# Kernel optimization log

Hardware: AMD Instinct MI355X
Metric: run time of the kernel (lower is better)

Reference implementation:

```python
import jax, jax.numpy as jnp
import numpy as np

D_MODEL = 1024
N_HEADS = 16
HEAD_DIM = D_MODEL // N_HEADS
D_FF = 4 * D_MODEL


def _layernorm(x, g, b, eps=1e-5):
    mu = jnp.mean(x, axis=-1, keepdims=True)
    var = jnp.var(x, axis=-1, keepdims=True)
    return (x - mu) * jax.lax.rsqrt(var + eps) * g + b


def setup_inputs() -> dict:
    key = jax.random.key(0)
    ks = jax.random.split(key, 12)
    s = lambda fan_in: 1.0 / np.sqrt(fan_in)
    x = jax.random.normal(ks[0], (2, 2048, D_MODEL), dtype=jnp.float32)
    return {
        "x": x,
        "ln1_g": jnp.ones((D_MODEL,), jnp.float32),
        "ln1_b": jnp.zeros((D_MODEL,), jnp.float32),
        "w_qkv": jax.random.uniform(ks[1], (D_MODEL, 3 * D_MODEL), jnp.float32, -s(D_MODEL), s(D_MODEL)),
        "b_qkv": jax.random.uniform(ks[2], (3 * D_MODEL,), jnp.float32, -s(D_MODEL), s(D_MODEL)),
        "w_out": jax.random.uniform(ks[3], (D_MODEL, D_MODEL), jnp.float32, -s(D_MODEL), s(D_MODEL)),
        "b_out": jax.random.uniform(ks[4], (D_MODEL,), jnp.float32, -s(D_MODEL), s(D_MODEL)),
        "ln2_g": jnp.ones((D_MODEL,), jnp.float32),
        "ln2_b": jnp.zeros((D_MODEL,), jnp.float32),
        "w_ff1": jax.random.uniform(ks[5], (D_MODEL, D_FF), jnp.float32, -s(D_MODEL), s(D_MODEL)),
        "b_ff1": jax.random.uniform(ks[6], (D_FF,), jnp.float32, -s(D_MODEL), s(D_MODEL)),
        "w_ff2": jax.random.uniform(ks[7], (D_FF, D_MODEL), jnp.float32, -s(D_FF), s(D_FF)),
        "b_ff2": jax.random.uniform(ks[8], (D_MODEL,), jnp.float32, -s(D_FF), s(D_FF)),
    }


def reference(x, ln1_g, ln1_b, w_qkv, b_qkv, w_out, b_out,
              ln2_g, ln2_b, w_ff1, b_ff1, w_ff2, b_ff2):
    B, T, C = x.shape
    # --- pre-LN causal self-attention + residual ---
    h = _layernorm(x, ln1_g, ln1_b)
    qkv = h @ w_qkv + b_qkv                                  # [B,T,3C]
    qkv = qkv.reshape(B, T, 3, N_HEADS, HEAD_DIM)
    q, k, v = qkv[:, :, 0], qkv[:, :, 1], qkv[:, :, 2]       # [B,T,H,Dh]
    scores = jnp.einsum("bthd,bshd->bhts", q, k) / np.sqrt(HEAD_DIM).astype(np.float32)
    causal = jnp.tril(jnp.ones((T, T), dtype=bool))
    scores = jnp.where(causal, scores, -jnp.inf)
    weights = jax.nn.softmax(scores, axis=-1)                # [B,H,T,T]
    attn = jnp.einsum("bhts,bshd->bthd", weights, v).reshape(B, T, C)
    x = x + attn @ w_out + b_out
    # --- pre-LN GELU FFN + residual ---
    h = _layernorm(x, ln2_g, ln2_b)
    h = jax.nn.gelu(h @ w_ff1 + b_ff1, approximate=False)    # torch GELU = erf
    x = x + h @ w_ff2 + b_ff2
    return x
```

## Files before the change

### kernel.cpp

```cpp
#include <hip/hip_runtime.h>
#include <hip/hip_bf16.h>
#include <math.h>

#define TSEQ 2048
#define BATCH 2
#define CDIM 1024
#define NH 16
#define HD 64
#define DFF 4096
#define ROWS (BATCH*TSEQ)

typedef __attribute__((ext_vector_type(4))) float f32x4;
typedef __attribute__((ext_vector_type(8))) short bf16x8;
typedef __attribute__((ext_vector_type(4))) unsigned short u16x4;

__device__ __forceinline__ void gload_lds16(const void* g, void* l) {
    void* gv = const_cast<void*>(g);
    __builtin_amdgcn_global_load_lds((__attribute__((address_space(1))) void*)gv,
                                     (__attribute__((address_space(3))) void*)l, 16, 0, 0);
}

__device__ __forceinline__ unsigned short f2bf(float f) {
    unsigned int u = __float_as_uint(f);
    return (unsigned short)((u + 0x7FFFu + ((u >> 16) & 1u)) >> 16);
}
__device__ __forceinline__ float bf2f(unsigned short u) {
    return __uint_as_float((unsigned int)u << 16);
}
__device__ __forceinline__ unsigned int cvt_pk_bf16(float lo, float hi) {
    unsigned int r;
    asm("v_cvt_pk_bf16_f32 %0, %1, %2" : "=v"(r) : "v"(lo), "v"(hi));
    return r;
}
__device__ __forceinline__ float fast_gelu(float v) {
    float u = fmaf(0.044715f * v * v, v, v);
    float e = __expf(-1.5957691216057308f * u);
    return v * __builtin_amdgcn_rcpf(1.0f + e);
}

__global__ __launch_bounds__(256) void ln_kernel(const float* __restrict__ x,
                                                 const float* __restrict__ g,
                                                 const float* __restrict__ b,
                                                 unsigned short* __restrict__ out) {
    int row = blockIdx.x;
    int tid = threadIdx.x;
    const float* xr = x + (size_t)row * CDIM;
    float4 v = *(const float4*)(xr + tid * 4);
    float s  = v.x + v.y + v.z + v.w;
    float s2 = v.x*v.x + v.y*v.y + v.z*v.z + v.w*v.w;
    #pragma unroll
    for (int off = 32; off >= 1; off >>= 1) {
        s  += __shfl_down(s, off);
        s2 += __shfl_down(s2, off);
    }
    __shared__ float red[8];
    int wid = tid >> 6, lane = tid & 63;
    if (lane == 0) { red[wid] = s; red[wid + 4] = s2; }
    __syncthreads();
    float ts  = red[0] + red[1] + red[2] + red[3];
    float ts2 = red[4] + red[5] + red[6] + red[7];
    float mu  = ts * (1.0f / CDIM);
    float var = ts2 * (1.0f / CDIM) - mu * mu;
    float rstd = rsqrtf(var + 1e-5f);
    float4 gv = *(const float4*)(g + tid * 4);
    float4 bv = *(const float4*)(b + tid * 4);
    unsigned short o4[4];
    o4[0] = f2bf((v.x - mu) * rstd * gv.x + bv.x);
    o4[1] = f2bf((v.y - mu) * rstd * gv.y + bv.y);
    o4[2] = f2bf((v.z - mu) * rstd * gv.z + bv.z);
    o4[3] = f2bf((v.w - mu) * rstd * gv.w + bv.w);
    *(u16x4*)(out + (size_t)row * CDIM + tid * 4) = *(u16x4*)o4;
}

__global__ __launch_bounds__(256) void transpose_cast_kernel(const float* __restrict__ W,
                                                             unsigned short* __restrict__ Wt,
                                                             int K, int N) {
    __shared__ float T[64][65];
    int tid = threadIdx.x;
    int n0 = blockIdx.x * 64, k0 = blockIdx.y * 64;
    int kr = tid >> 4;
    int nc = (tid & 15) * 4;
    #pragma unroll
    for (int i = 0; i < 4; ++i) {
        float4 v = *(const float4*)&W[(size_t)(k0 + kr + i*16) * N + (n0 + nc)];
        T[kr + i*16][nc + 0] = v.x;
        T[kr + i*16][nc + 1] = v.y;
        T[kr + i*16][nc + 2] = v.z;
        T[kr + i*16][nc + 3] = v.w;
    }
    __syncthreads();
    int n  = tid >> 2;
    int kb = (tid & 3) * 16;
    unsigned short tmp[16];
    #pragma unroll
    for (int i = 0; i < 16; ++i) tmp[i] = f2bf(T[kb + i][n]);
    unsigned short* dst = Wt + (size_t)(n0 + n) * K + (k0 + kb);
    *(int4*)dst       = *(int4*)&tmp[0];
    *(int4*)(dst + 8) = *(int4*)&tmp[8];
}

__global__ __launch_bounds__(256) void kvfrag_kernel(const unsigned short* __restrict__ qkv,
                                                     unsigned short* __restrict__ kfrag,
                                                     unsigned short* __restrict__ vfrag) {
    __shared__ unsigned short Kt[64][72];
    __shared__ unsigned short Vt[64][72];
    const int tid = threadIdx.x;
    const int j  = blockIdx.x;
    const int bh = blockIdx.y;
    const int b = bh >> 4, h = bh & 15;
    {
        const int r  = tid >> 2;
        const int c0 = (tid & 3) * 16;
        const unsigned short* src = qkv + ((size_t)(b * TSEQ + j * 64 + r)) * 3072 + 1024 + h * 64 + c0;
        bf16x8 k0 = *(const bf16x8*)src;
        bf16x8 k1 = *(const bf16x8*)(src + 8);
        bf16x8 v0 = *(const bf16x8*)(src + 1024);
        bf16x8 v1 = *(const bf16x8*)(src + 1032);
        *(bf16x8*)&Kt[r][c0]     = k0;
        *(bf16x8*)&Kt[r][c0 + 8] = k1;
        *(bf16x8*)&Vt[r][c0]     = v0;
        *(bf16x8*)&Vt[r][c0 + 8] = v1;
    }
    __syncthreads();
    const int l  = tid & 63;
    const int qd = tid >> 6;
    const size_t tbase = ((size_t)(bh * 32 + j)) * 8 * 512;
    #pragma unroll
    for (int pass = 0; pass < 2; ++pass) {
        const int kc = qd + pass * 4;
        const int sb = kc >> 1, g = kc & 1;
        bf16x8 kv = *(const bf16x8*)&Kt[sb * 16 + (l & 15)][g * 32 + (l >> 4) * 8];
        *(bf16x8*)(kfrag + tbase + kc * 512 + l * 8) = kv;

        const int vc = qd + pass * 4;
        const int kb = vc >> 2, db = vc & 3;
        unsigned short tmp[8];
        #pragma unroll
        for (int i = 0; i < 8; ++i)
            tmp[i] = Vt[kb * 32 + (l >> 4) * 8 + i][db * 16 + (l & 15)];
        *(bf16x8*)(vfrag + tbase + vc * 512 + l * 8) = *(bf16x8*)tmp;
    }
}

template<int EPI>
__global__ __launch_bounds__(256) void gemm_kernel(const unsigned short* __restrict__ A,
                                                   const unsigned short* __restrict__ Bt,
                                                   const float* __restrict__ bias,
                                                   const float* __restrict__ res,
                                                   void* __restrict__ Cout,
                                                   int M, int N, int K, int nbx, int rpx) {
    __shared__ __align__(16) unsigned short As[3 * 4096];
    __shared__ __align__(16) unsigned short Bs[3 * 4096];
    const int tid = threadIdx.x;
    const int l   = tid & 63;
    const int w   = tid >> 6;
    const int wr  = (w >> 1) * 64;
    const int wc  = (w & 1) * 64;
    const int lin = blockIdx.x;
    const int xcd = lin & 7;
    const int idx = lin >> 3;
    const long brow = (long)(xcd * rpx + idx / nbx) * 128;
    const long bcol = (long)(idx % nbx) * 128;

    const int srow = tid >> 2;
    const int schk = ((tid & 3) ^ ((srow >> 1) & 3)) * 8;
    const unsigned short* gA = A  + (size_t)(brow + srow) * K + schk;
    const unsigned short* gB = Bt + (size_t)(bcol + srow) * K + schk;

    f32x4 acc[4][4];
    #pragma unroll
    for (int m = 0; m < 4; ++m)
        #pragma unroll
        for (int n = 0; n < 4; ++n) acc[m][n] = (f32x4){0.f, 0.f, 0.f, 0.f};

    #define STAGE128(buf, koff_)                                                       \
        do {                                                                           \
            unsigned short* lA_ = As + (buf) * 4096 + tid * 8;                         \
            unsigned short* lB_ = Bs + (buf) * 4096 + tid * 8;                         \
            gload_lds16(gA + (koff_), lA_);                                            \
            gload_lds16(gA + (size_t)64 * K + (koff_), lA_ + 2048);                    \
            gload_lds16(gB + (koff_), lB_);                                            \
            gload_lds16(gB + (size_t)64 * K + (koff_), lB_ + 2048);                    \
        } while (0)

    STAGE128(0, 0);
    STAGE128(1, 32);

    int cur = 0;
    for (int k0 = 0; k0 < K; k0 += 32) {
        if (k0 + 32 < K) asm volatile("s_waitcnt vmcnt(4)" ::: "memory");
        else             asm volatile("s_waitcnt vmcnt(0)" ::: "memory");
        __builtin_amdgcn_s_barrier();
        asm volatile("" ::: "memory");

        const unsigned short* cA = As + cur * 4096 + (wr >> 6) * 2048;
        const unsigned short* cB = Bs + cur * 4096 + (wc >> 6) * 2048;
        const int koff = ((l >> 4) ^ (((l & 15) >> 1) & 3)) * 8;
        bf16x8 af[4], bf[4];
        #pragma unroll
        for (int m = 0; m < 4; ++m)
            af[m] = *(const bf16x8*)&cA[(m * 16 + (l & 15)) * 32 + koff];
        #pragma unroll
        for (int n = 0; n < 4; ++n)
            bf[n] = *(const bf16x8*)&cB[(n * 16 + (l & 15)) * 32 + koff];
        __builtin_amdgcn_s_setprio(1);
        #pragma unroll
        for (int m = 0; m < 4; ++m)
            #pragma unroll
            for (int n = 0; n < 4; ++n)
                acc[m][n] = __builtin_amdgcn_mfma_f32_16x16x32_bf16(af[m], bf[n], acc[m][n], 0, 0, 0);
        __builtin_amdgcn_s_setprio(0);

        if (k0 + 64 < K) {
            int nxt = cur + 2; if (nxt >= 3) nxt -= 3;
            STAGE128(nxt, k0 + 64);
        }
        cur = cur + 1; if (cur == 3) cur = 0;
    }
    #undef STAGE128

    #pragma unroll
    for (int m = 0; m < 4; ++m) {
        const int rown = wr + m * 16 + (l >> 4) * 4;
        #pragma unroll
        for (int n = 0; n < 4; ++n) {
            const long col = bcol + wc + n * 16 + (l & 15);
            const float bb = bias[col];
            #pragma unroll
            for (int r = 0; r < 4; ++r) {
                const long row = brow + rown + r;
                float v = acc[m][n][r] + bb;
                if (EPI == 1) {
                    v += res[row * N + col];
                    ((float*)Cout)[row * N + col] = v;
                } else if (EPI == 2) {
                    ((unsigned short*)Cout)[row * N + col] = f2bf(fast_gelu(v));
                } else {
                    ((unsigned short*)Cout)[row * N + col] = f2bf(v);
                }
            }
        }
    }
}

template<int EPI>
__global__ __launch_bounds__(256) void gemm64_kernel(const unsigned short* __restrict__ A,
                                                     const unsigned short* __restrict__ Bt,
                                                     const float* __restrict__ bias,
                                                     const float* __restrict__ res,
                                                     void* __restrict__ Cout,
                                                     int M, int N, int K, int nbx, int rpx) {
    __shared__ __align__(16) unsigned short As[3 * 64 * 64];
    __shared__ __align__(16) unsigned short Bs[3 * 128 * 64];
    const int tid = threadIdx.x;
    const int l   = tid & 63;
    const int w   = tid >> 6;
    const int wr  = (w >> 1) * 32;
    const int wc  = (w & 1) * 64;
    const int lin = blockIdx.x;
    const int xcd = lin & 7;
    const int idx = lin >> 3;
    const long brow = (long)(xcd * rpx + idx / nbx) * 64;
    const long bcol = (long)(idx % nbx) * 128;

    const int srow = tid >> 3;
    const int schk = ((tid & 7) ^ (srow & 7)) * 8;
    const unsigned short* gA = A  + (size_t)(brow + srow) * K + schk;
    const unsigned short* gB = Bt + (size_t)(bcol + srow) * K + schk;

    f32x4 acc[2][4];
    #pragma unroll
    for (int m = 0; m < 2; ++m)
        #pragma unroll
        for (int n = 0; n < 4; ++n) acc[m][n] = (f32x4){0.f, 0.f, 0.f, 0.f};

    #define STAGE64(buf, koff_)                                                        \
        do {                                                                           \
            unsigned short* lA_ = As + (buf) * 4096 + tid * 8;                         \
            unsigned short* lB_ = Bs + (buf) * 8192 + tid * 8;                         \
            _Pragma("unroll")                                                          \
            for (int p = 0; p < 2; ++p)                                                \
                gload_lds16(gA + (size_t)(32 * p) * K + (koff_), lA_ + p * 2048);      \
            _Pragma("unroll")                                                          \
            for (int p = 0; p < 4; ++p)                                                \
                gload_lds16(gB + (size_t)(32 * p) * K + (koff_), lB_ + p * 2048);      \
        } while (0)

    STAGE64(0, 0);
    STAGE64(1, 64);

    int cur = 0;
    for (int k0 = 0; k0 < K; k0 += 64) {
        if (k0 + 64 < K) asm volatile("s_waitcnt vmcnt(6)" ::: "memory");
        else             asm volatile("s_waitcnt vmcnt(0)" ::: "memory");
        __builtin_amdgcn_s_barrier();
        asm volatile("" ::: "memory");

        const unsigned short* cA = As + cur * 4096;
        const unsigned short* cB = Bs + cur * 8192;
        #pragma unroll
        for (int gg = 0; gg < 2; ++gg) {
            const int koff = ((gg * 4 + (l >> 4)) ^ (l & 7)) * 8;
            bf16x8 af[2], bf[4];
            #pragma unroll
            for (int m = 0; m < 2; ++m)
                af[m] = *(const bf16x8*)&cA[(wr + m * 16 + (l & 15)) * 64 + koff];
            #pragma unroll
            for (int n = 0; n < 4; ++n)
                bf[n] = *(const bf16x8*)&cB[(wc + n * 16 + (l & 15)) * 64 + koff];
            __builtin_amdgcn_s_setprio(1);
            #pragma unroll
            for (int m = 0; m < 2; ++m)
                #pragma unroll
                for (int n = 0; n < 4; ++n)
                    acc[m][n] = __builtin_amdgcn_mfma_f32_16x16x32_bf16(af[m], bf[n], acc[m][n], 0, 0, 0);
            __builtin_amdgcn_s_setprio(0);
        }

        if (k0 + 128 < K) {
            int nxt = cur + 2; if (nxt >= 3) nxt -= 3;
            STAGE64(nxt, k0 + 128);
        }
        cur = cur + 1; if (cur == 3) cur = 0;
    }
    #undef STAGE64

    #pragma unroll
    for (int m = 0; m < 2; ++m) {
        const int rown = wr + m * 16 + (l >> 4) * 4;
        #pragma unroll
        for (int n = 0; n < 4; ++n) {
            const long col = bcol + wc + n * 16 + (l & 15);
            const float bb = bias[col];
            #pragma unroll
            for (int r = 0; r < 4; ++r) {
                const long row = brow + rown + r;
                float v = acc[m][n][r] + bb;
                if (EPI == 1) {
                    v += res[row * N + col];
                    ((float*)Cout)[row * N + col] = v;
                } else if (EPI == 2) {
                    ((unsigned short*)Cout)[row * N + col] = f2bf(fast_gelu(v));
                } else {
                    ((unsigned short*)Cout)[row * N + col] = f2bf(v);
                }
            }
        }
    }
}

#define QSCALE 0.18033688011112042f
__global__ __launch_bounds__(64) void attn_kernel(const unsigned short* __restrict__ qkv,
                                                  const unsigned short* __restrict__ kfrag,
                                                  const unsigned short* __restrict__ vfrag,
                                                  unsigned short* __restrict__ out) {
    __shared__ __align__(16) unsigned short Ps[16 * 128];

    const int l    = threadIdx.x;
    const int q    = l & 15;
    const int g    = l >> 4;
    const int lin  = blockIdx.x;
    const int xcd  = lin & 7;
    const int rest = lin >> 3;
    const int h    = xcd + 8 * (rest & 1);
    const int b    = (rest >> 1) & 1;
    const int strip = 127 - (rest >> 2);
    const int jmax  = strip >> 2;
    const size_t rowbase = (size_t)b * TSEQ;
    const int bh = b * NH + h;
    const int qglob = strip * 16 + q;

    const unsigned short* kfb = kfrag + (size_t)bh * 32 * 8 * 512;
    const unsigned short* vfb = vfrag + (size_t)bh * 32 * 8 * 512;

    bf16x8 aq0, aq1;
    {
        const unsigned short* qp = qkv + (rowbase + qglob) * 3072 + h * 64 + g * 8;
        bf16x8 t0 = *(const bf16x8*)qp;
        bf16x8 t1 = *(const bf16x8*)(qp + 32);
        #pragma unroll
        for (int i = 0; i < 8; ++i) {
            aq0[i] = (short)f2bf(bf2f((unsigned short)t0[i]) * QSCALE);
            aq1[i] = (short)f2bf(bf2f((unsigned short)t1[i]) * QSCALE);
        }
    }

    float mrow = -INFINITY, lrow = 0.f;
    f32x4 o[4];
    #pragma unroll
    for (int d = 0; d < 4; ++d) o[d] = (f32x4){0.f, 0.f, 0.f, 0.f};

    for (int j = 0; j + 1 <= jmax; j += 2) {
        const bool diag2 = (j + 1 == jmax);

        bf16x8 kf[16];
        #pragma unroll
        for (int t = 0; t < 2; ++t)
            #pragma unroll
            for (int sb = 0; sb < 4; ++sb) {
                const unsigned short* kp = kfb + (size_t)((j + t) * 8 + sb * 2) * 512 + l * 8;
                kf[t * 8 + sb * 2]     = *(const bf16x8*)kp;
                kf[t * 8 + sb * 2 + 1] = *(const bf16x8*)(kp + 512);
            }

        f32x4 sf[8];
        __builtin_amdgcn_s_setprio(1);
        #pragma unroll
        for (int t = 0; t < 2; ++t)
            #pragma unroll
            for (int sb = 0; sb < 4; ++sb) {
                f32x4 acc = (f32x4){0.f, 0.f, 0.f, 0.f};
                acc = __builtin_amdgcn_mfma_f32_16x16x32_bf16(kf[t*8 + sb*2],     aq0, acc, 0, 0, 0);
                acc = __builtin_amdgcn_mfma_f32_16x16x32_bf16(kf[t*8 + sb*2 + 1], aq1, acc, 0, 0, 0);
                sf[t*4 + sb] = acc;
            }
        __builtin_amdgcn_s_setprio(0);

        bf16x8 vf[16];
        #pragma unroll
        for (int kb = 0; kb < 4; ++kb)
            #pragma unroll
            for (int db = 0; db < 4; ++db)
                vf[kb * 4 + db] = *(const bf16x8*)(vfb + (size_t)((j + (kb >> 1)) * 8 + (kb & 1) * 4 + db) * 512 + l * 8);

        if (diag2) {
            #pragma unroll
            for (int sb = 0; sb < 4; ++sb) {
                const int sg = (j + 1) * 64 + sb * 16 + 4 * g;
                #pragma unroll
                for (int r = 0; r < 4; ++r)
                    if (sg + r > qglob) sf[4 + sb][r] = -INFINITY;
            }
        }

        f32x4 mv = sf[0];
        #pragma unroll
        for (int i = 1; i < 8; ++i)
            #pragma unroll
            for (int r = 0; r < 4; ++r) mv[r] = fmaxf(mv[r], sf[i][r]);
        float mloc = fmaxf(fmaxf(mv[0], mv[1]), fmaxf(mv[2], mv[3]));
        mloc = fmaxf(mloc, __shfl_xor(mloc, 16));
        mloc = fmaxf(mloc, __shfl_xor(mloc, 32));
        const float mn = fmaxf(mrow, mloc);
        const float alpha = exp2f(mrow - mn);
        mrow = mn;

        float psum = 0.f;
        #pragma unroll
        for (int i = 0; i < 8; ++i) {
            const int t = i >> 2, sb = i & 3;
            float p0 = exp2f(sf[i][0] - mn);
            float p1 = exp2f(sf[i][1] - mn);
            float p2 = exp2f(sf[i][2] - mn);
            float p3 = exp2f(sf[i][3] - mn);
            psum += (p0 + p1) + (p2 + p3);
            unsigned int pk0 = cvt_pk_bf16(p0, p1);
            unsigned int pk1 = cvt_pk_bf16(p2, p3);
            const int c16 = (t * 8 + sb * 2 + (g >> 1)) ^ (q & 7);
            *(uint2*)((char*)Ps + q * 256 + c16 * 16 + (g & 1) * 8) = make_uint2(pk0, pk1);
        }
        psum += __shfl_xor(psum, 16);
        psum += __shfl_xor(psum, 32);
        lrow = lrow * alpha + psum;

        float al[4];
        #pragma unroll
        for (int r = 0; r < 4; ++r) al[r] = __shfl(alpha, g * 4 + r);
        #pragma unroll
        for (int d = 0; d < 4; ++d)
            #pragma unroll
            for (int r = 0; r < 4; ++r) o[d][r] *= al[r];

        __builtin_amdgcn_s_setprio(1);
        #pragma unroll
        for (int kb = 0; kb < 4; ++kb) {
            const int c16 = (kb * 4 + g) ^ (q & 7);
            bf16x8 pa = *(const bf16x8*)((const char*)Ps + q * 256 + c16 * 16);
            #pragma unroll
            for (int db = 0; db < 4; ++db)
                o[db] = __builtin_amdgcn_mfma_f32_16x16x32_bf16(pa, vf[kb * 4 + db], o[db], 0, 0, 0);
        }
        __builtin_amdgcn_s_setprio(0);
    }

    if ((jmax & 1) == 0) {
        const int j = jmax;
        bf16x8 kf[8];
        #pragma unroll
        for (int sb = 0; sb < 4; ++sb) {
            const unsigned short* kp = kfb + (size_t)(j * 8 + sb * 2) * 512 + l * 8;
            kf[sb * 2]     = *(const bf16x8*)kp;
            kf[sb * 2 + 1] = *(const bf16x8*)(kp + 512);
        }
        f32x4 sf[4];
        __builtin_amdgcn_s_setprio(1);
        #pragma unroll
        for (int sb = 0; sb < 4; ++sb) {
            f32x4 acc = (f32x4){0.f, 0.f, 0.f, 0.f};
            acc = __builtin_amdgcn_mfma_f32_16x16x32_bf16(kf[sb*2],     aq0, acc, 0, 0, 0);
            acc = __builtin_amdgcn_mfma_f32_16x16x32_bf16(kf[sb*2 + 1], aq1, acc, 0, 0, 0);
            sf[sb] = acc;
        }
        __builtin_amdgcn_s_setprio(0);

        bf16x8 vf[8];
        #pragma unroll
        for (int kb = 0; kb < 2; ++kb)
            #pragma unroll
            for (int db = 0; db < 4; ++db)
                vf[kb * 4 + db] = *(const bf16x8*)(vfb + (size_t)(j * 8 + kb * 4 + db) * 512 + l * 8);

        #pragma unroll
        for (int sb = 0; sb < 4; ++sb) {
            const int sg = j * 64 + sb * 16 + 4 * g;
            #pragma unroll
            for (int r = 0; r < 4; ++r)
                if (sg + r > qglob) sf[sb][r] = -INFINITY;
        }

        f32x4 mv = sf[0];
        #pragma unroll
        for (int i = 1; i < 4; ++i)
            #pragma unroll
            for (int r = 0; r < 4; ++r) mv[r] = fmaxf(mv[r], sf[i][r]);
        float mloc = fmaxf(fmaxf(mv[0], mv[1]), fmaxf(mv[2], mv[3]));
        mloc = fmaxf(mloc, __shfl_xor(mloc, 16));
        mloc = fmaxf(mloc, __shfl_xor(mloc, 32));
        const float mn = fmaxf(mrow, mloc);
        const float alpha = exp2f(mrow - mn);
        mrow = mn;

        float psum = 0.f;
        #pragma unroll
        for (int sb = 0; sb < 4; ++sb) {
            float p0 = exp2f(sf[sb][0] - mn);
            float p1 = exp2f(sf[sb][1] - mn);
            float p2 = exp2f(sf[sb][2] - mn);
            float p3 = exp2f(sf[sb][3] - mn);
            psum += (p0 + p1) + (p2 + p3);
            unsigned int pk0 = cvt_pk_bf16(p0, p1);
            unsigned int pk1 = cvt_pk_bf16(p2, p3);
            const int c16 = (sb * 2 + (g >> 1)) ^ (q & 7);
            *(uint2*)((char*)Ps + q * 256 + c16 * 16 + (g & 1) * 8) = make_uint2(pk0, pk1);
        }
        psum += __shfl_xor(psum, 16);
        psum += __shfl_xor(psum, 32);
        lrow = lrow * alpha + psum;

        float al[4];
        #pragma unroll
        for (int r = 0; r < 4; ++r) al[r] = __shfl(alpha, g * 4 + r);
        #pragma unroll
        for (int d = 0; d < 4; ++d)
            #pragma unroll
            for (int r = 0; r < 4; ++r) o[d][r] *= al[r];

        __builtin_amdgcn_s_setprio(1);
        #pragma unroll
        for (int kb = 0; kb < 2; ++kb) {
            const int c16 = (kb * 4 + g) ^ (q & 7);
            bf16x8 pa = *(const bf16x8*)((const char*)Ps + q * 256 + c16 * 16);
            #pragma unroll
            for (int db = 0; db < 4; ++db)
                o[db] = __builtin_amdgcn_mfma_f32_16x16x32_bf16(pa, vf[kb * 4 + db], o[db], 0, 0, 0);
        }
        __builtin_amdgcn_s_setprio(0);
    }

    float linv[4];
    #pragma unroll
    for (int r = 0; r < 4; ++r) linv[r] = 1.0f / __shfl(lrow, g * 4 + r);
    #pragma unroll
    for (int r = 0; r < 4; ++r) {
        const size_t rb = (rowbase + strip * 16 + g * 4 + r) * (size_t)CDIM + h * 64 + q;
        #pragma unroll
        for (int d = 0; d < 4; ++d)
            out[rb + d * 16] = f2bf(o[d][r] * linv[r]);
    }
}

extern "C" void kernel_launch(void* const* d_in, const int* in_sizes, int n_in,
                              void* d_out, int out_size, void* d_ws, size_t ws_size,
                              hipStream_t stream) {
    const float* x     = (const float*)d_in[0];
    const float* ln1_g = (const float*)d_in[1];
    const float* ln1_b = (const float*)d_in[2];
    const float* w_qkv = (const float*)d_in[3];
    const float* b_qkv = (const float*)d_in[4];
    const float* w_out = (const float*)d_in[5];
    const float* b_out = (const float*)d_in[6];
    const float* ln2_g = (const float*)d_in[7];
    const float* ln2_b = (const float*)d_in[8];
    const float* w_ff1 = (const float*)d_in[9];
    const float* b_ff1 = (const float*)d_in[10];
    const float* w_ff2 = (const float*)d_in[11];
    const float* b_ff2 = (const float*)d_in[12];
    float* out = (float*)d_out;

    char* wsb = (char*)d_ws;
    unsigned short* h_bf    = (unsigned short*)(wsb);
    unsigned short* qkv_bf  = (unsigned short*)(wsb + 8ll  * 1024 * 1024);
    unsigned short* attn_bf = (unsigned short*)(wsb + 32ll * 1024 * 1024);
    float*          x1      = (float*)         (wsb + 40ll * 1024 * 1024);
    unsigned short* kfrag   = (unsigned short*)(wsb + 40ll * 1024 * 1024);
    unsigned short* vfrag   = (unsigned short*)(wsb + 48ll * 1024 * 1024);
    unsigned short* wqkvT   = (unsigned short*)(wsb + 56ll * 1024 * 1024);
    unsigned short* woutT   = (unsigned short*)(wsb + 62ll * 1024 * 1024);
    unsigned short* wff1T   = (unsigned short*)(wsb + 64ll * 1024 * 1024);
    unsigned short* wff2T   = (unsigned short*)(wsb + 72ll * 1024 * 1024);
    unsigned short* ff1_bf  = (unsigned short*)(wsb + 8ll  * 1024 * 1024);

    transpose_cast_kernel<<<dim3(48, 16), 256, 0, stream>>>(w_qkv, wqkvT, 1024, 3072);
    transpose_cast_kernel<<<dim3(16, 16), 256, 0, stream>>>(w_out, woutT, 1024, 1024);
    transpose_cast_kernel<<<dim3(64, 16), 256, 0, stream>>>(w_ff1, wff1T, 1024, 4096);
    transpose_cast_kernel<<<dim3(16, 64), 256, 0, stream>>>(w_ff2, wff2T, 4096, 1024);

    ln_kernel<<<ROWS, 256, 0, stream>>>(x, ln1_g, ln1_b, h_bf);
    gemm_kernel<0><<<768, 256, 0, stream>>>(h_bf, wqkvT, b_qkv, nullptr, qkv_bf, ROWS, 3072, 1024, 24, 4);
    kvfrag_kernel<<<dim3(32, 32), 256, 0, stream>>>(qkv_bf, kfrag, vfrag);
    attn_kernel<<<4096, 64, 0, stream>>>(qkv_bf, kfrag, vfrag, attn_bf);
    gemm64_kernel<1><<<512, 256, 0, stream>>>(attn_bf, woutT, b_out, x, x1, ROWS, 1024, 1024, 8, 8);
    ln_kernel<<<ROWS, 256, 0, stream>>>(x1, ln2_g, ln2_b, h_bf);
    gemm_kernel<2><<<1024, 256, 0, stream>>>(h_bf, wff1T, b_ff1, nullptr, ff1_bf, ROWS, 4096, 1024, 32, 4);
    gemm64_kernel<1><<<512, 256, 0, stream>>>(ff1_bf, wff2T, b_ff2, x1, (float*)out, ROWS, 1024, 4096, 8, 8);
}
```

Baseline: 240.0 us.

## Process two adjacent query strips per attention wavefront to share K/V fragment loads

Each attention workgroup now handles two consecutive 16-row query strips instead of one, so the K and V fragments loaded per key block are reused for both strips. The grid is halved to 2048 single-wave blocks. The aim is to cut global K/V load traffic per query and interleave independent softmax and MFMA work from the two strips. In exchange, register pressure roughly doubles for accumulators and scores, and fewer waves are in flight to hide latency.

```diff
diff --git a/kernel.cpp b/kernel.cpp
--- a/kernel.cpp
+++ b/kernel.cpp
@@ -349,12 +349,114 @@
     }
 }
 
+__device__ __forceinline__ void sm8(f32x4 (&sf)[8], float& mrow, float& lrow,
+                                    f32x4 (&o)[4], char* ps, int q, int g) {
+    f32x4 mv = sf[0];
+    #pragma unroll
+    for (int i = 1; i < 8; ++i)
+        #pragma unroll
+        for (int r = 0; r < 4; ++r) mv[r] = fmaxf(mv[r], sf[i][r]);
+    float mloc = fmaxf(fmaxf(mv[0], mv[1]), fmaxf(mv[2], mv[3]));
+    mloc = fmaxf(mloc, __shfl_xor(mloc, 16));
+    mloc = fmaxf(mloc, __shfl_xor(mloc, 32));
+    const float mn = fmaxf(mrow, mloc);
+    const float alpha = exp2f(mrow - mn);
+    mrow = mn;
+    float psum = 0.f;
+    #pragma unroll
+    for (int i = 0; i < 8; ++i) {
+        const int t = i >> 2, sb = i & 3;
+        float p0 = exp2f(sf[i][0] - mn);
+        float p1 = exp2f(sf[i][1] - mn);
+        float p2 = exp2f(sf[i][2] - mn);
+        float p3 = exp2f(sf[i][3] - mn);
+        psum += (p0 + p1) + (p2 + p3);
+        unsigned int pk0 = cvt_pk_bf16(p0, p1);
+        unsigned int pk1 = cvt_pk_bf16(p2, p3);
+        const int c16 = (t * 8 + sb * 2 + (g >> 1)) ^ (q & 7);
+        *(uint2*)(ps + q * 256 + c16 * 16 + (g & 1) * 8) = make_uint2(pk0, pk1);
+    }
+    psum += __shfl_xor(psum, 16);
+    psum += __shfl_xor(psum, 32);
+    lrow = lrow * alpha + psum;
+    float al[4];
+    #pragma unroll
+    for (int r = 0; r < 4; ++r) al[r] = __shfl(alpha, g * 4 + r);
+    #pragma unroll
+    for (int d = 0; d < 4; ++d)
+        #pragma unroll
+        for (int r = 0; r < 4; ++r) o[d][r] *= al[r];
+}
+__device__ __forceinline__ void pv8(const char* ps, const bf16x8 (&vf)[16],
+                                    f32x4 (&o)[4], int q, int g) {
+    __builtin_amdgcn_s_setprio(1);
+    #pragma unroll
+    for (int kb = 0; kb < 4; ++kb) {
+        const int c16 = (kb * 4 + g) ^ (q & 7);
+        bf16x8 pa = *(const bf16x8*)(ps + q * 256 + c16 * 16);
+        #pragma unroll
+        for (int db = 0; db < 4; ++db)
+            o[db] = __builtin_amdgcn_mfma_f32_16x16x32_bf16(pa, vf[kb * 4 + db], o[db], 0, 0, 0);
+    }
+    __builtin_amdgcn_s_setprio(0);
+}
+__device__ __forceinline__ void sm4(f32x4 (&sf)[4], float& mrow, float& lrow,
+                                    f32x4 (&o)[4], char* ps, int q, int g) {
+    f32x4 mv = sf[0];
+    #pragma unroll
+    for (int i = 1; i < 4; ++i)
+        #pragma unroll
+        for (int r = 0; r < 4; ++r) mv[r] = fmaxf(mv[r], sf[i][r]);
+    float mloc = fmaxf(fmaxf(mv[0], mv[1]), fmaxf(mv[2], mv[3]));
+    mloc = fmaxf(mloc, __shfl_xor(mloc, 16));
+    mloc = fmaxf(mloc, __shfl_xor(mloc, 32));
+    const float mn = fmaxf(mrow, mloc);
+    const float alpha = exp2f(mrow - mn);
+    mrow = mn;
+    float psum = 0.f;
+    #pragma unroll
+    for (int sb = 0; sb < 4; ++sb) {
+        float p0 = exp2f(sf[sb][0] - mn);
+        float p1 = exp2f(sf[sb][1] - mn);
+        float p2 = exp2f(sf[sb][2] - mn);
+        float p3 = exp2f(sf[sb][3] - mn);
+        psum += (p0 + p1) + (p2 + p3);
+        unsigned int pk0 = cvt_pk_bf16(p0, p1);
+        unsigned int pk1 = cvt_pk_bf16(p2, p3);
+        const int c16 = (sb * 2 + (g >> 1)) ^ (q & 7);
+        *(uint2*)(ps + q * 256 + c16 * 16 + (g & 1) * 8) = make_uint2(pk0, pk1);
+    }
+    psum += __shfl_xor(psum, 16);
+    psum += __shfl_xor(psum, 32);
+    lrow = lrow * alpha + psum;
+    float al[4];
+    #pragma unroll
+    for (int r = 0; r < 4; ++r) al[r] = __shfl(alpha, g * 4 + r);
+    #pragma unroll
+    for (int d = 0; d < 4; ++d)
+        #pragma unroll
+        for (int r = 0; r < 4; ++r) o[d][r] *= al[r];
+}
+__device__ __forceinline__ void pv4(const char* ps, const bf16x8 (&vf)[8],
+                                    f32x4 (&o)[4], int q, int g) {
+    __builtin_amdgcn_s_setprio(1);
+    #pragma unroll
+    for (int kb = 0; kb < 2; ++kb) {
+        const int c16 = (kb * 4 + g) ^ (q & 7);
+        bf16x8 pa = *(const bf16x8*)(ps + q * 256 + c16 * 16);
+        #pragma unroll
+        for (int db = 0; db < 4; ++db)
+            o[db] = __builtin_amdgcn_mfma_f32_16x16x32_bf16(pa, vf[kb * 4 + db], o[db], 0, 0, 0);
+    }
+    __builtin_amdgcn_s_setprio(0);
+}
+
 #define QSCALE 0.18033688011112042f
 __global__ __launch_bounds__(64) void attn_kernel(const unsigned short* __restrict__ qkv,
                                                   const unsigned short* __restrict__ kfrag,
                                                   const unsigned short* __restrict__ vfrag,
                                                   unsigned short* __restrict__ out) {
-    __shared__ __align__(16) unsigned short Ps[16 * 128];
+    __shared__ __align__(16) unsigned short Ps[2 * 16 * 128];
 
     const int l    = threadIdx.x;
     const int q    = l & 15;
@@ -364,31 +466,44 @@
     const int rest = lin >> 3;
     const int h    = xcd + 8 * (rest & 1);
     const int b    = (rest >> 1) & 1;
-    const int strip = 127 - (rest >> 2);
-    const int jmax  = strip >> 2;
+    const int p    = 63 - (rest >> 2);
+    const int s0   = 2 * p, s1 = 2 * p + 1;
+    const int jmax = s0 >> 2;
     const size_t rowbase = (size_t)b * TSEQ;
     const int bh = b * NH + h;
-    const int qglob = strip * 16 + q;
+    const int qgA = s0 * 16 + q;
+    const int qgB = s1 * 16 + q;
+    char* psA = (char*)Ps;
+    char* psB = (char*)Ps + 4096;
 
     const unsigned short* kfb = kfrag + (size_t)bh * 32 * 8 * 512;
     const unsigned short* vfb = vfrag + (size_t)bh * 32 * 8 * 512;
 
-    bf16x8 aq0, aq1;
+    bf16x8 aqA0, aqA1, aqB0, aqB1;
     {
-        const unsigned short* qp = qkv + (rowbase + qglob) * 3072 + h * 64 + g * 8;
-        bf16x8 t0 = *(const bf16x8*)qp;
-        bf16x8 t1 = *(const bf16x8*)(qp + 32);
+        const unsigned short* qpA = qkv + (rowbase + qgA) * 3072 + h * 64 + g * 8;
+        const unsigned short* qpB = qkv + (rowbase + qgB) * 3072 + h * 64 + g * 8;
+        bf16x8 tA0 = *(const bf16x8*)qpA;
+        bf16x8 tA1 = *(const bf16x8*)(qpA + 32);
+        bf16x8 tB0 = *(const bf16x8*)qpB;
+        bf16x8 tB1 = *(const bf16x8*)(qpB + 32);
         #pragma unroll
         for (int i = 0; i < 8; ++i) {
-            aq0[i] = (short)f2bf(bf2f((unsigned short)t0[i]) * QSCALE);
-            aq1[i] = (short)f2bf(bf2f((unsigned short)t1[i]) * QSCALE);
-        }
-    }
-
-    float mrow = -INFINITY, lrow = 0.f;
-    f32x4 o[4];
-    #pragma unroll
-    for (int d = 0; d < 4; ++d) o[d] = (f32x4){0.f, 0.f, 0.f, 0.f};
+            aqA0[i] = (short)f2bf(bf2f((unsigned short)tA0[i]) * QSCALE);
+            aqA1[i] = (short)f2bf(bf2f((unsigned short)tA1[i]) * QSCALE);
+            aqB0[i] = (short)f2bf(bf2f((unsigned short)tB0[i]) * QSCALE);
+            aqB1[i] = (short)f2bf(bf2f((unsigned short)tB1[i]) * QSCALE);
+        }
+    }
+
+    float mrowA = -INFINITY, lrowA = 0.f;
+    float mrowB = -INFINITY, lrowB = 0.f;
+    f32x4 oA[4], oB[4];
+    #pragma unroll
+    for (int d = 0; d < 4; ++d) {
+        oA[d] = (f32x4){0.f, 0.f, 0.f, 0.f};
+        oB[d] = (f32x4){0.f, 0.f, 0.f, 0.f};
+    }
 
     for (int j = 0; j + 1 <= jmax; j += 2) {
         const bool diag2 = (j + 1 == jmax);
@@ -403,84 +518,62 @@
                 kf[t * 8 + sb * 2 + 1] = *(const bf16x8*)(kp + 512);
             }
 
-        f32x4 sf[8];
+        f32x4 sa[8];
         __builtin_amdgcn_s_setprio(1);
         #pragma unroll
         for (int t = 0; t < 2; ++t)
             #pragma unroll
             for (int sb = 0; sb < 4; ++sb) {
                 f32x4 acc = (f32x4){0.f, 0.f, 0.f, 0.f};
-                acc = __builtin_amdgcn_mfma_f32_16x16x32_bf16(kf[t*8 + sb*2],     aq0, acc, 0, 0, 0);
-                acc = __builtin_amdgcn_mfma_f32_16x16x32_bf16(kf[t*8 + sb*2 + 1], aq1, acc, 0, 0, 0);
-                sf[t*4 + sb] = acc;
+                acc = __builtin_amdgcn_mfma_f32_16x16x32_bf16(kf[t*8 + sb*2],     aqA0, acc, 0, 0, 0);
+                acc = __builtin_amdgcn_mfma_f32_16x16x32_bf16(kf[t*8 + sb*2 + 1], aqA1, acc, 0, 0, 0);
+                sa[t*4 + sb] = acc;
             }
         __builtin_amdgcn_s_setprio(0);
-
-        bf16x8 vf[16];
-        #pragma unroll
-        for (int kb = 0; kb < 4; ++kb)
-            #pragma unroll
-            for (int db = 0; db < 4; ++db)
-                vf[kb * 4 + db] = *(const bf16x8*)(vfb + (size_t)((j + (kb >> 1)) * 8 + (kb & 1) * 4 + db) * 512 + l * 8);
-
         if (diag2) {
             #pragma unroll
             for (int sb = 0; sb < 4; ++sb) {
                 const int sg = (j + 1) * 64 + sb * 16 + 4 * g;
                 #pragma unroll
                 for (int r = 0; r < 4; ++r)
-                    if (sg + r > qglob) sf[4 + sb][r] = -INFINITY;
+                    if (sg + r > qgA) sa[4 + sb][r] = -INFINITY;
             }
         }
-
-        f32x4 mv = sf[0];
-        #pragma unroll
-        for (int i = 1; i < 8; ++i)
-            #pragma unroll
-            for (int r = 0; r < 4; ++r) mv[r] = fmaxf(mv[r], sf[i][r]);
-        float mloc = fmaxf(fmaxf(mv[0], mv[1]), fmaxf(mv[2], mv[3]));
-        mloc = fmaxf(mloc, __shfl_xor(mloc, 16));
-        mloc = fmaxf(mloc, __shfl_xor(mloc, 32));
-        const float mn = fmaxf(mrow, mloc);
-        const float alpha = exp2f(mrow - mn);
-        mrow = mn;
-
-        float psum = 0.f;
-        #pragma unroll
-        for (int i = 0; i < 8; ++i) {
-            const int t = i >> 2, sb = i & 3;
-            float p0 = exp2f(sf[i][0] - mn);
-            float p1 = exp2f(sf[i][1] - mn);
-            float p2 = exp2f(sf[i][2] - mn);
-            float p3 = exp2f(sf[i][3] - mn);
-            psum += (p0 + p1) + (p2 + p3);
-            unsigned int pk0 = cvt_pk_bf16(p0, p1);
-            unsigned int pk1 = cvt_pk_bf16(p2, p3);
-            const int c16 = (t * 8 + sb * 2 + (g >> 1)) ^ (q & 7);
-            *(uint2*)((char*)Ps + q * 256 + c16 * 16 + (g & 1) * 8) = make_uint2(pk0, pk1);
-        }
-        psum += __shfl_xor(psum, 16);
-        psum += __shfl_xor(psum, 32);
-        lrow = lrow * alpha + psum;
-
-        float al[4];
-        #pragma unroll
-        for (int r = 0; r < 4; ++r) al[r] = __shfl(alpha, g * 4 + r);
-        #pragma unroll
-        for (int d = 0; d < 4; ++d)
-            #pragma unroll
-            for (int r = 0; r < 4; ++r) o[d][r] *= al[r];
-
+        sm8(sa, mrowA, lrowA, oA, psA, q, g);
+
+        f32x4 sb8[8];
         __builtin_amdgcn_s_setprio(1);
         #pragma unroll
-        for (int kb = 0; kb < 4; ++kb) {
-            const int c16 = (kb * 4 + g) ^ (q & 7);
-            bf16x8 pa = *(const bf16x8*)((const char*)Ps + q * 256 + c16 * 16);
+        for (int t = 0; t < 2; ++t)
+            #pragma unroll
+            for (int sb = 0; sb < 4; ++sb) {
+                f32x4 acc = (f32x4){0.f, 0.f, 0.f, 0.f};
+                acc = __builtin_amdgcn_mfma_f32_16x16x32_bf16(kf[t*8 + sb*2],     aqB0, acc, 0, 0, 0);
+                acc = __builtin_amdgcn_mfma_f32_16x16x32_bf16(kf[t*8 + sb*2 + 1], aqB1, acc, 0, 0, 0);
+                sb8[t*4 + sb] = acc;
+            }
+        __builtin_amdgcn_s_setprio(0);
+
+        bf16x8 vf[16];
+        #pragma unroll
+        for (int kb = 0; kb < 4; ++kb)
             #pragma unroll
             for (int db = 0; db < 4; ++db)
-                o[db] = __builtin_amdgcn_mfma_f32_16x16x32_bf16(pa, vf[kb * 4 + db], o[db], 0, 0, 0);
-        }
-        __builtin_amdgcn_s_setprio(0);
+                vf[kb * 4 + db] = *(const bf16x8*)(vfb + (size_t)((j + (kb >> 1)) * 8 + (kb & 1) * 4 + db) * 512 + l * 8);
+
+        if (diag2) {
+            #pragma unroll
+            for (int sb = 0; sb < 4; ++sb) {
+                const int sg = (j + 1) * 64 + sb * 16 + 4 * g;
+                #pragma unroll
+                for (int r = 0; r < 4; ++r)
+                    if (sg + r > qgB) sb8[4 + sb][r] = -INFINITY;
+            }
+        }
+        sm8(sb8, mrowB, lrowB, oB, psB, q, g);
+
+        pv8(psA, vf, oA, q, g);
+        pv8(psB, vf, oB, q, g);
     }
 
     if ((jmax & 1) == 0) {
@@ -492,14 +585,33 @@
             kf[sb * 2]     = *(const bf16x8*)kp;
             kf[sb * 2 + 1] = *(const bf16x8*)(kp + 512);
         }
-        f32x4 sf[4];
+        f32x4 sa[4];
         __builtin_amdgcn_s_setprio(1);
         #pragma unroll
         for (int sb = 0; sb < 4; ++sb) {
             f32x4 acc = (f32x4){0.f, 0.f, 0.f, 0.f};
-            acc = __builtin_amdgcn_mfma_f32_16x16x32_bf16(kf[sb*2],     aq0, acc, 0, 0, 0);
-            acc = __builtin_amdgcn_mfma_f32_16x16x32_bf16(kf[sb*2 + 1], aq1, acc, 0, 0, 0);
-            sf[sb] = acc;
+            acc = __builtin_amdgcn_mfma_f32_16x16x32_bf16(kf[sb*2],     aqA0, acc, 0, 0, 0);
+            acc = __builtin_amdgcn_mfma_f32_16x16x32_bf16(kf[sb*2 + 1], aqA1, acc, 0, 0, 0);
+            sa[sb] = acc;
+        }
+        __builtin_amdgcn_s_setprio(0);
+        #pragma unroll
+        for (int sb = 0; sb < 4; ++sb) {
+            const int sg = j * 64 + sb * 16 + 4 * g;
+            #pragma unroll
+            for (int r = 0; r < 4; ++r)
+                if (sg + r > qgA) sa[sb][r] = -INFINITY;
+        }
+        sm4(sa, mrowA, lrowA, oA, psA, q, g);
+
+        f32x4 sb4[4];
+        __builtin_amdgcn_s_setprio(1);
+        #pragma unroll
+        for (int sb = 0; sb < 4; ++sb) {
+            f32x4 acc = (f32x4){0.f, 0.f, 0.f, 0.f};
+            acc = __builtin_amdgcn_mfma_f32_16x16x32_bf16(kf[sb*2],     aqB0, acc, 0, 0, 0);
+            acc = __builtin_amdgcn_mfma_f32_16x16x32_bf16(kf[sb*2 + 1], aqB1, acc, 0, 0, 0);
+            sb4[sb] = acc;
         }
         __builtin_amdgcn_s_setprio(0);
 
@@ -515,67 +627,29 @@
             const int sg = j * 64 + sb * 16 + 4 * g;
             #pragma unroll
             for (int r = 0; r < 4; ++r)
-                if (sg + r > qglob) sf[sb][r] = -INFINITY;
-        }
-
-        f32x4 mv = sf[0];
-        #pragma unroll
-        for (int i = 1; i < 4; ++i)
-            #pragma unroll
-            for (int r = 0; r < 4; ++r) mv[r] = fmaxf(mv[r], sf[i][r]);
-        float mloc = fmaxf(fmaxf(mv[0], mv[1]), fmaxf(mv[2], mv[3]));
-        mloc = fmaxf(mloc, __shfl_xor(mloc, 16));
-        mloc = fmaxf(mloc, __shfl_xor(mloc, 32));
-        const float mn = fmaxf(mrow, mloc);
-        const float alpha = exp2f(mrow - mn);
-        mrow = mn;
-
-        float psum = 0.f;
-        #pragma unroll
-        for (int sb = 0; sb < 4; ++sb) {
-            float p0 = exp2f(sf[sb][0] - mn);
-            float p1 = exp2f(sf[sb][1] - mn);
-            float p2 = exp2f(sf[sb][2] - mn);
-            float p3 = exp2f(sf[sb][3] - mn);
-            psum += (p0 + p1) + (p2 + p3);
-            unsigned int pk0 = cvt_pk_bf16(p0, p1);
-            unsigned int pk1 = cvt_pk_bf16(p2, p3);
-            const int c16 = (sb * 2 + (g >> 1)) ^ (q & 7);
-            *(uint2*)((char*)Ps + q * 256 + c16 * 16 + (g & 1) * 8) = make_uint2(pk0, pk1);
-        }
-        psum += __shfl_xor(psum, 16);
-        psum += __shfl_xor(psum, 32);
-        lrow = lrow * alpha + psum;
-
-        float al[4];
-        #pragma unroll
-        for (int r = 0; r < 4; ++r) al[r] = __shfl(alpha, g * 4 + r);
-        #pragma unroll
-        for (int d = 0; d < 4; ++d)
-            #pragma unroll
-            for (int r = 0; r < 4; ++r) o[d][r] *= al[r];
-
-        __builtin_amdgcn_s_setprio(1);
-        #pragma unroll
-        for (int kb = 0; kb < 2; ++kb) {
-            const int c16 = (kb * 4 + g) ^ (q & 7);
-            bf16x8 pa = *(const bf16x8*)((const char*)Ps + q * 256 + c16 * 16);
-            #pragma unroll
-            for (int db = 0; db < 4; ++db)
-                o[db] = __builtin_amdgcn_mfma_f32_16x16x32_bf16(pa, vf[kb * 4 + db], o[db], 0, 0, 0);
-        }
-        __builtin_amdgcn_s_setprio(0);
-    }
-
-    float linv[4];
-    #pragma unroll
-    for (int r = 0; r < 4; ++r) linv[r] = 1.0f / __shfl(lrow, g * 4 + r);
+                if (sg + r > qgB) sb4[sb][r] = -INFINITY;
+        }
+        sm4(sb4, mrowB, lrowB, oB, psB, q, g);
+
+        pv4(psA, vf, oA, q, g);
+        pv4(psB, vf, oB, q, g);
+    }
+
+    float linvA[4], linvB[4];
     #pragma unroll
     for (int r = 0; r < 4; ++r) {
-        const size_t rb = (rowbase + strip * 16 + g * 4 + r) * (size_t)CDIM + h * 64 + q;
-        #pragma unroll
-        for (int d = 0; d < 4; ++d)
-            out[rb + d * 16] = f2bf(o[d][r] * linv[r]);
+        linvA[r] = 1.0f / __shfl(lrowA, g * 4 + r);
+        linvB[r] = 1.0f / __shfl(lrowB, g * 4 + r);
+    }
+    #pragma unroll
+    for (int r = 0; r < 4; ++r) {
+        const size_t rbA = (rowbase + s0 * 16 + g * 4 + r) * (size_t)CDIM + h * 64 + q;
+        const size_t rbB = (rowbase + s1 * 16 + g * 4 + r) * (size_t)CDIM + h * 64 + q;
+        #pragma unroll
+        for (int d = 0; d < 4; ++d) {
+            out[rbA + d * 16] = f2bf(oA[d][r] * linvA[r]);
+            out[rbB + d * 16] = f2bf(oB[d][r] * linvB[r]);
+        }
     }
 }
 
@@ -618,7 +692,7 @@
     ln_kernel<<<ROWS, 256, 0, stream>>>(x, ln1_g, ln1_b, h_bf);
     gemm_kernel<0><<<768, 256, 0, stream>>>(h_bf, wqkvT, b_qkv, nullptr, qkv_bf, ROWS, 3072, 1024, 24, 4);
     kvfrag_kernel<<<dim3(32, 32), 256, 0, stream>>>(qkv_bf, kfrag, vfrag);
-    attn_kernel<<<4096, 64, 0, stream>>>(qkv_bf, kfrag, vfrag, attn_bf);
+    attn_kernel<<<2048, 64, 0, stream>>>(qkv_bf, kfrag, vfrag, attn_bf);
     gemm64_kernel<1><<<512, 256, 0, stream>>>(attn_bf, woutT, b_out, x, x1, ROWS, 1024, 1024, 8, 8);
     ln_kernel<<<ROWS, 256, 0, stream>>>(x1, ln2_g, ln2_b, h_bf);
     gemm_kernel<2><<<1024, 256, 0, stream>>>(h_bf, wff1T, b_ff1, nullptr, ff1_bf, ROWS, 4096, 1024, 32, 4);
```

Measured after the change: 246.8 us. 2.8% more time.
